# Optimization experiments

Measured on AMD Instinct MI355X. Metric: run time of the kernel, lower is better.

## Reference

```python
import jax, jax.numpy as jnp
import numpy as np

N = 50000      # nodes
E = 800000     # edges (avg degree 16)
HID = 64       # hidden / out_channels per head (concat=False)
EDIM = 3       # edge_dim
H = 4          # heads
C = 64         # per-head channels (== hidden since concat=False mean)
L = 2          # ode_layers
NEG_SLOPE = 0.2
LN_EPS = 1e-5


def setup_inputs() -> dict:
    key = jax.random.key(0)
    ks = jax.random.split(key, 12)
    h = jax.random.normal(ks[0], (N, HID), dtype=jnp.float32)
    edge_index = jax.random.randint(ks[1], (2, E), 0, N, dtype=jnp.int64)
    edge_attr = jax.random.normal(ks[2], (E, EDIM), dtype=jnp.float32)
    t = jnp.zeros((), dtype=jnp.float32)
    s = 1.0 / np.sqrt(HID)
    lin_W = jax.random.normal(ks[3], (L, H * C, HID), dtype=jnp.float32) * s
    lin_W = lin_W.at[L - 1].mul(0.1)  # mimics gats[-1].lin.weight.mul_(0.1)
    lin_edge_W = jax.random.normal(ks[4], (L, H * C, EDIM), dtype=jnp.float32) * (1.0 / np.sqrt(EDIM))
    att_src = jax.random.normal(ks[5], (L, H, C), dtype=jnp.float32) * s
    att_dst = jax.random.normal(ks[6], (L, H, C), dtype=jnp.float32) * s
    att_edge = jax.random.normal(ks[7], (L, H, C), dtype=jnp.float32) * s
    bias = jnp.zeros((L, C), dtype=jnp.float32)
    ln_gamma = jnp.ones((L, HID), dtype=jnp.float32)
    ln_beta = jnp.zeros((L, HID), dtype=jnp.float32)
    return {"t": t, "h": h, "edge_index": edge_index, "edge_attr": edge_attr,
            "lin_W": lin_W, "lin_edge_W": lin_edge_W, "att_src": att_src,
            "att_dst": att_dst, "att_edge": att_edge, "bias": bias,
            "ln_gamma": ln_gamma, "ln_beta": ln_beta}


def _gat_layer(z, src, dst, lin_W, lin_edge_W, att_src, att_dst, att_edge,
               bias, edge_attr):
    n = z.shape[0]
    x = (z @ lin_W.T).reshape(n, H, C)                      # [N,H,C]
    a_src = (x * att_src).sum(-1)                            # [N,H]
    a_dst = (x * att_dst).sum(-1)                            # [N,H]
    e = (edge_attr @ lin_edge_W.T).reshape(-1, H, C)         # [E,H,C]
    a_e = (e * att_edge).sum(-1)                             # [E,H]
    alpha = jax.nn.leaky_relu(a_src[src] + a_dst[dst] + a_e, NEG_SLOPE)
    # segment-softmax over incoming edges of each destination node
    amax = jax.ops.segment_max(alpha, dst, num_segments=n)
    amax = jnp.where(jnp.isfinite(amax), amax, 0.0)
    ex = jnp.exp(alpha - amax[dst])                          # [E,H]
    denom = jax.ops.segment_sum(ex, dst, num_segments=n)
    w = ex / (denom[dst] + 1e-16)
    msg = jax.ops.segment_sum(w[:, :, None] * x[src], dst, num_segments=n)
    return msg.mean(axis=1) + bias                           # [N,C] (concat=False)


def reference(t, h, edge_index, edge_attr, lin_W, lin_edge_W, att_src,
              att_dst, att_edge, bias, ln_gamma, ln_beta):
    src, dst = edge_index[0], edge_index[1]
    z = h
    for i in range(L):
        out = _gat_layer(z, src, dst, lin_W[i], lin_edge_W[i], att_src[i],
                         att_dst[i], att_edge[i], bias[i], edge_attr)
        mu = out.mean(-1, keepdims=True)
        var = ((out - mu) ** 2).mean(-1, keepdims=True)
        ln = (out - mu) / jnp.sqrt(var + LN_EPS) * ln_gamma[i] + ln_beta[i]
        z = jax.nn.silu(ln)
    return z
```

## Files before the change

### kernel.cpp

```cpp
#include <hip/hip_runtime.h>
#include <math.h>

#define NN 50000
#define NE 800000
#define NEG_SLOPE 0.2f
#define LN_EPS 1e-5f
#define SROW 264

typedef unsigned short ushort_t;
typedef unsigned int uint_t;
typedef __attribute__((ext_vector_type(8))) short bf16x8;
typedef __attribute__((ext_vector_type(4))) float f32x4;

__device__ __forceinline__ float bf2f(ushort_t u) {
    return __uint_as_float(((uint_t)u) << 16);
}
__device__ __forceinline__ ushort_t f2bf(float f) {
    uint_t b = __float_as_uint(f);
    uint_t r = (b + 0x7fffu + ((b >> 16) & 1u)) >> 16;
    return (ushort_t)r;
}
__device__ __forceinline__ float ldx(const void* p, size_t i, int isbf) {
    return isbf ? bf2f(((const ushort_t*)p)[i]) : ((const float*)p)[i];
}
__device__ __forceinline__ int clampN(int v) {
    return v < 0 ? 0 : (v >= NN ? NN - 1 : v);
}
__device__ __forceinline__ int ld_src(const int* ei, int e, int f64) {
    return clampN(f64 ? ei[2 * e] : ei[e]);
}
__device__ __forceinline__ int ld_dst(const int* ei, int e, int f64) {
    return clampN(f64 ? ei[2 * NE + 2 * e] : ei[NE + e]);
}
__device__ __forceinline__ int sniff_isbf(const void* hptr) {
    const ushort_t* hu = (const ushort_t*)hptr;
    int bf = 1;
    for (int i = 0; i < 512; i += 2) {
        uint_t ex = (hu[i] >> 7) & 0xFFu;
        if (ex > 0x8Cu) bf = 0;
    }
    return bf;
}
__device__ __forceinline__ int sniff_f64(const int* ei) {
    return (ei[1] == 0 && ei[3] == 0 && ei[5] == 0 && ei[7] == 0) ? 1 : 0;
}

__global__ __launch_bounds__(256) void setup(
    const void* __restrict__ lin_W, const void* __restrict__ lin_edge_W,
    const void* __restrict__ att_src, const void* __restrict__ att_dst,
    const void* __restrict__ att_edge, const void* __restrict__ h_in,
    const int* __restrict__ ei, float* __restrict__ Mbuf,
    ushort_t* __restrict__ wext, ushort_t* __restrict__ hbf,
    int* __restrict__ deg, int* __restrict__ flags) {
    int tid = threadIdx.x, lane = tid & 63;
    int nthreads = gridDim.x * 256;
    int gtid = blockIdx.x * 256 + tid;
    __shared__ int s_isbf;
    if (tid == 0) s_isbf = sniff_isbf(h_in);
    __syncthreads();
    int isbf = s_isbf;
    if (gtid == 0) {
        flags[0] = sniff_f64(ei);
        flags[1] = isbf;
    }
    for (int i = gtid; i < NN; i += nthreads) deg[i] = 0;
    if (blockIdx.x == 0) {
        for (int rep = 0; rep < 2; ++rep) {
            int idx = rep * 256 + tid;
            int l = idx >> 8, hc = idx & 255;
            float ae = ldx(att_edge, l * 256 + hc, isbf);
            size_t b3 = ((size_t)l * 256 + hc) * 3;
            float q0 = ae * ldx(lin_edge_W, b3 + 0, isbf);
            float q1 = ae * ldx(lin_edge_W, b3 + 1, isbf);
            float q2 = ae * ldx(lin_edge_W, b3 + 2, isbf);
            for (int off = 32; off > 0; off >>= 1) {
                q0 += __shfl_down(q0, off);
                q1 += __shfl_down(q1, off);
                q2 += __shfl_down(q2, off);
            }
            if (lane == 0) {
                int h = (idx >> 6) & 3;
                Mbuf[(l * 4 + h) * 3 + 0] = q0;
                Mbuf[(l * 4 + h) * 3 + 1] = q1;
                Mbuf[(l * 4 + h) * 3 + 2] = q2;
            }
        }
    }
    for (int idx = gtid; idx < 2 * 272 * 64; idx += nthreads) {
        int d = idx & 63;
        int row = (idx >> 6) % 272;
        int l = idx / (272 * 64);
        float v = 0.f;
        if (row < 256) {
            v = ldx(lin_W, ((size_t)l * 256 + row) * 64 + d, isbf);
        } else if (row < 264) {
            int h = (row - 256) & 3;
            const void* att = (row < 260) ? att_src : att_dst;
            for (int c = 0; c < 64; ++c) {
                v += ldx(lin_W, ((size_t)l * 256 + h * 64 + c) * 64 + d, isbf) *
                     ldx(att, l * 256 + h * 64 + c, isbf);
            }
        }
        wext[((size_t)l * 272 + row) * 64 + d] = f2bf(v);
    }
    if (!isbf) {
        for (int i = gtid; i < NN * 64; i += nthreads)
            hbf[i] = f2bf(((const float*)h_in)[i]);
    }
}


__global__ void csr_hist_pos(const int* __restrict__ ei, int* __restrict__ deg,
                             int* __restrict__ pos, const int* __restrict__ flags) {
    int e = blockIdx.x * 256 + threadIdx.x;
    if (e >= NE) return;
    pos[e] = atomicAdd(&deg[ld_dst(ei, e, flags[0])], 1);
}

__global__ __launch_bounds__(1024) void csr_scan1(const int* __restrict__ deg,
                                                  int* __restrict__ rowptr,
                                                  int* __restrict__ bsum) {
    __shared__ int sh[1024];
    int i = blockIdx.x * 1024 + threadIdx.x;
    int v = (i < NN) ? deg[i] : 0;
    sh[threadIdx.x] = v;
    __syncthreads();
    for (int off = 1; off < 1024; off <<= 1) {
        int t = (threadIdx.x >= off) ? sh[threadIdx.x - off] : 0;
        __syncthreads();
        sh[threadIdx.x] += t;
        __syncthreads();
    }
    if (i < NN) rowptr[i] = sh[threadIdx.x] - v;
    if (threadIdx.x == 1023) bsum[blockIdx.x] = sh[1023];
}

__global__ __launch_bounds__(1024) void csr_scan23(int* __restrict__ rowptr,
                                                   const int* __restrict__ bsum,
                                                   int nb) {
    __shared__ int off_sh;
    int tid = threadIdx.x;
    if (tid < 64) {
        int v = (tid < blockIdx.x && tid < nb) ? bsum[tid] : 0;
        for (int off = 32; off > 0; off >>= 1) v += __shfl_down(v, off);
        if (tid == 0) off_sh = v;
    }
    __syncthreads();
    int i = blockIdx.x * 1024 + tid;
    if (i < NN) rowptr[i] += off_sh;
    if (i == 0) rowptr[NN] = NE;
}

__global__ void csr_fill(const int* __restrict__ ei, const void* __restrict__ edge_attr,
                         const int* __restrict__ rowptr, const int* __restrict__ pos,
                         float4* __restrict__ edata, const int* __restrict__ flags) {
    int e = blockIdx.x * 256 + threadIdx.x;
    if (e >= NE) return;
    int f64 = flags[0], isbf = flags[1];
    int s = ld_src(ei, e, f64), d = ld_dst(ei, e, f64);
    float4 ed;
    ed.x = ldx(edge_attr, (size_t)e * 3 + 0, isbf);
    ed.y = ldx(edge_attr, (size_t)e * 3 + 1, isbf);
    ed.z = ldx(edge_attr, (size_t)e * 3 + 2, isbf);
    ed.w = __int_as_float(s);
    edata[rowptr[d] + pos[e]] = ed;
}


__global__ __launch_bounds__(256) void node_linear(
    const void* __restrict__ h_in, const ushort_t* __restrict__ hbf,
    const ushort_t* __restrict__ zbuf, const ushort_t* __restrict__ wext,
    ushort_t* __restrict__ xb, float* __restrict__ a_src, float* __restrict__ a_dst,
    const int* __restrict__ flags, int layer) {
    __shared__ __align__(16) ushort_t st_all[4 * 16 * SROW];
    int isbf = flags[1];
    int tid = threadIdx.x, wv = tid >> 6, lane = tid & 63;
    int q = lane >> 4, mi = lane & 15;
    const ushort_t* zsrc = (layer == 0) ? (isbf ? (const ushort_t*)h_in : hbf) : zbuf;
    const ushort_t* wl = wext + (size_t)layer * 272 * 64;
    bf16x8 wf[34];
#pragma unroll
    for (int t = 0; t < 17; ++t) {
        const ushort_t* wrow = wl + (size_t)(t * 16 + mi) * 64;
        wf[2 * t]     = *(const bf16x8*)(wrow + q * 8);
        wf[2 * t + 1] = *(const bf16x8*)(wrow + 32 + q * 8);
    }
    ushort_t* st = st_all + wv * 16 * SROW;
    int gwave = blockIdx.x * 4 + wv, nwaves = gridDim.x * 4;
    for (int tile = gwave; tile < NN / 16; tile += nwaves) {
        int mbase = tile * 16, mynode = mbase + mi;
        const ushort_t* zrow = zsrc + (size_t)mynode * 64;
        bf16x8 b0 = *(const bf16x8*)(zrow + q * 8);
        bf16x8 b1 = *(const bf16x8*)(zrow + 32 + q * 8);
#pragma unroll
        for (int t = 0; t < 17; ++t) {
            f32x4 acc = {0.f, 0.f, 0.f, 0.f};
            acc = __builtin_amdgcn_mfma_f32_16x16x32_bf16(wf[2 * t], b0, acc, 0, 0, 0);
            acc = __builtin_amdgcn_mfma_f32_16x16x32_bf16(wf[2 * t + 1], b1, acc, 0, 0, 0);
            if (t < 16) {
                ushort4 pk;
                pk.x = f2bf(acc[0]);
                pk.y = f2bf(acc[1]);
                pk.z = f2bf(acc[2]);
                pk.w = f2bf(acc[3]);
                *(ushort4*)(st + mi * SROW + t * 16 + q * 4) = pk;
            } else {
                float4 av;
                av.x = acc[0]; av.y = acc[1]; av.z = acc[2]; av.w = acc[3];
                if (q == 0) *(float4*)(a_src + (size_t)mynode * 4) = av;
                else if (q == 1) *(float4*)(a_dst + (size_t)mynode * 4) = av;
            }
        }
        for (int nn = 0; nn < 16; ++nn) {
            int node = mbase + nn;
            ushort4 pk;
            pk.x = st[nn * SROW + lane];
            pk.y = st[nn * SROW + 64 + lane];
            pk.z = st[nn * SROW + 128 + lane];
            pk.w = st[nn * SROW + 192 + lane];
            *(ushort4*)(xb + (size_t)node * 256 + lane * 4) = pk;
        }
    }
}

__global__ __launch_bounds__(256) void node_aggregate(
    const int* __restrict__ rowptr, const float4* __restrict__ edata,
    const float* __restrict__ a_src, const float* __restrict__ a_dst,
    const ushort_t* __restrict__ xb, const float* __restrict__ Mbuf,
    const void* __restrict__ bias, const void* __restrict__ gamma,
    const void* __restrict__ beta, ushort_t* __restrict__ zout,
    void* __restrict__ outp, const int* __restrict__ flags, int layer, int last) {
    __shared__ float4 wsh[4][64];
    __shared__ int ssh[4][64];
    int isbf = flags[1];
    int wv = threadIdx.x >> 6;
    int lane = threadIdx.x & 63;
    int n = blockIdx.x * 4 + wv;
    float M[12];
#pragma unroll
    for (int i = 0; i < 12; ++i) M[i] = Mbuf[layer * 12 + i];
    float4 ad = *(const float4*)(a_dst + (size_t)n * 4);
    int start = rowptr[n], end = rowptr[n + 1];
    float acc0 = 0.f, acc1 = 0.f, acc2 = 0.f, acc3 = 0.f;
    float den0 = 0.f, den1 = 0.f, den2 = 0.f, den3 = 0.f;
    for (int cb = start; cb < end; cb += 64) {
        int m = end - cb;
        if (m > 64) m = 64;
        if (lane < m) {
            float4 ed = edata[cb + lane];
            int s = __float_as_int(ed.w);
            float4 as4 = *(const float4*)(a_src + (size_t)s * 4);
            float t0 = as4.x + ad.x + ed.x * M[0] + ed.y * M[1] + ed.z * M[2];
            float t1 = as4.y + ad.y + ed.x * M[3] + ed.y * M[4] + ed.z * M[5];
            float t2 = as4.z + ad.z + ed.x * M[6] + ed.y * M[7] + ed.z * M[8];
            float t3 = as4.w + ad.w + ed.x * M[9] + ed.y * M[10] + ed.z * M[11];
            t0 = t0 > 0.f ? t0 : NEG_SLOPE * t0;
            t1 = t1 > 0.f ? t1 : NEG_SLOPE * t1;
            t2 = t2 > 0.f ? t2 : NEG_SLOPE * t2;
            t3 = t3 > 0.f ? t3 : NEG_SLOPE * t3;
            float4 ex;
            ex.x = __expf(fminf(t0, 80.f));
            ex.y = __expf(fminf(t1, 80.f));
            ex.z = __expf(fminf(t2, 80.f));
            ex.w = __expf(fminf(t3, 80.f));
            wsh[wv][lane] = ex;
            ssh[wv][lane] = s;
        }
        for (int j = 0; j < m; j += 4) {
            int j1 = j + 1 < m ? j + 1 : m - 1;
            int j2 = j + 2 < m ? j + 2 : m - 1;
            int j3 = j + 3 < m ? j + 3 : m - 1;
            int s0 = ssh[wv][j],  s1 = ssh[wv][j1];
            int s2 = ssh[wv][j2], s3 = ssh[wv][j3];
            float4 w0 = wsh[wv][j];
            float4 w1 = wsh[wv][j1];
            float4 w2 = wsh[wv][j2];
            float4 w3 = wsh[wv][j3];
            if (j + 1 >= m) w1 = make_float4(0.f, 0.f, 0.f, 0.f);
            if (j + 2 >= m) w2 = make_float4(0.f, 0.f, 0.f, 0.f);
            if (j + 3 >= m) w3 = make_float4(0.f, 0.f, 0.f, 0.f);
            ushort4 x0 = *(const ushort4*)(xb + (size_t)s0 * 256 + lane * 4);
            ushort4 x1 = *(const ushort4*)(xb + (size_t)s1 * 256 + lane * 4);
            ushort4 x2 = *(const ushort4*)(xb + (size_t)s2 * 256 + lane * 4);
            ushort4 x3 = *(const ushort4*)(xb + (size_t)s3 * 256 + lane * 4);
            acc0 += w0.x * bf2f(x0.x) + w1.x * bf2f(x1.x) +
                    w2.x * bf2f(x2.x) + w3.x * bf2f(x3.x);
            acc1 += w0.y * bf2f(x0.y) + w1.y * bf2f(x1.y) +
                    w2.y * bf2f(x2.y) + w3.y * bf2f(x3.y);
            acc2 += w0.z * bf2f(x0.z) + w1.z * bf2f(x1.z) +
                    w2.z * bf2f(x2.z) + w3.z * bf2f(x3.z);
            acc3 += w0.w * bf2f(x0.w) + w1.w * bf2f(x1.w) +
                    w2.w * bf2f(x2.w) + w3.w * bf2f(x3.w);
            den0 += w0.x + w1.x + w2.x + w3.x;
            den1 += w0.y + w1.y + w2.y + w3.y;
            den2 += w0.z + w1.z + w2.z + w3.z;
            den3 += w0.w + w1.w + w2.w + w3.w;
        }
    }
    float v = ldx(bias, layer * 64 + lane, isbf) +
              0.25f * (acc0 / (den0 + 1e-16f) + acc1 / (den1 + 1e-16f) +
                       acc2 / (den2 + 1e-16f) + acc3 / (den3 + 1e-16f));
    float sum = v;
    for (int off = 1; off < 64; off <<= 1) sum += __shfl_xor(sum, off);
    float mu = sum * (1.f / 64.f);
    float d = v - mu;
    float vv = d * d;
    for (int off = 1; off < 64; off <<= 1) vv += __shfl_xor(vv, off);
    float var = vv * (1.f / 64.f);
    float ln = d * rsqrtf(var + LN_EPS) * ldx(gamma, layer * 64 + lane, isbf) +
               ldx(beta, layer * 64 + lane, isbf);
    float sl = ln / (1.f + __expf(-ln));
    size_t idx = (size_t)n * 64 + lane;
    if (last) {
        if (isbf) ((ushort_t*)outp)[idx] = f2bf(sl);
        else      ((float*)outp)[idx] = sl;
    } else {
        zout[idx] = f2bf(sl);
    }
}

extern "C" void kernel_launch(void* const* d_in, const int* in_sizes, int n_in,
                              void* d_out, int out_size, void* d_ws, size_t ws_size,
                              hipStream_t stream) {
    int off = (in_sizes[0] == 1) ? 1 : 0;
    const void* h_in  = d_in[off + 0];
    const int*  ei    = (const int*)d_in[off + 1];
    const void* eattr = d_in[off + 2];
    const void* linW  = d_in[off + 3];
    const void* linEW = d_in[off + 4];
    const void* attS  = d_in[off + 5];
    const void* attD  = d_in[off + 6];
    const void* attE  = d_in[off + 7];
    const void* bias  = d_in[off + 8];
    const void* gamma = d_in[off + 9];
    const void* beta  = d_in[off + 10];

    char* w = (char*)d_ws;
    size_t o = 0;
    auto alloc = [&](size_t bytes) {
        void* q = w + o;
        o += (bytes + 255) & ~(size_t)255;
        return q;
    };
    int*    flags  = (int*)alloc(8);
    float*  Mbuf   = (float*)alloc(24 * 4);
    ushort_t* wext = (ushort_t*)alloc((size_t)2 * 272 * 64 * 2);
    float*  a_src  = (float*)alloc((size_t)NN * 4 * 4);
    float*  a_dst  = (float*)alloc((size_t)NN * 4 * 4);
    int*    rowptr = (int*)alloc((size_t)(NN + 1) * 4);
    int*    deg    = (int*)alloc((size_t)NN * 4);
    int*    pos    = (int*)alloc((size_t)NE * 4);
    int*    bsum   = (int*)alloc(256 * 4);
    ushort_t* zbuf = (ushort_t*)alloc((size_t)NN * 64 * 2);
    ushort_t* hbf  = (ushort_t*)alloc((size_t)NN * 64 * 2);
    ushort_t* xb   = (ushort_t*)alloc((size_t)NN * 256 * 2);
    float4* edata  = (float4*)alloc((size_t)NE * 16);

    int nb = (NN + 1023) / 1024;
    setup<<<256, 256, 0, stream>>>(linW, linEW, attS, attD, attE, h_in, ei,
                                   Mbuf, wext, hbf, deg, flags);
    csr_hist_pos<<<(NE + 255) / 256, 256, 0, stream>>>(ei, deg, pos, flags);
    csr_scan1<<<nb, 1024, 0, stream>>>(deg, rowptr, bsum);
    csr_scan23<<<nb, 1024, 0, stream>>>(rowptr, bsum, nb);
    csr_fill<<<(NE + 255) / 256, 256, 0, stream>>>(ei, eattr, rowptr, pos, edata, flags);

    for (int l = 0; l < 2; ++l) {
        node_linear<<<512, 256, 0, stream>>>(h_in, hbf, zbuf, wext, xb,
                                             a_src, a_dst, flags, l);
        node_aggregate<<<NN / 4, 256, 0, stream>>>(rowptr, edata, a_src, a_dst,
                                                   xb, Mbuf, bias, gamma, beta,
                                                   zbuf, d_out, flags, l, l == 1);
    }
}
```

Before: 329.9 us.

## Make node_aggregate lanes own one head's 4 contiguous channels

Changes the xb layout from channel-interleaved to head-major contiguous by writing rows with a vector LDS read. In node_aggregate, each lane now handles one head and 4 consecutive channels, so it needs one softmax weight per edge instead of four. The per-edge weights and pre-shifted source offsets are staged in LDS as grouped quads, read with vector loads, accumulated with FMAs, and the heads are reduced through cross-lane shuffles. This is meant to cut per-edge ALU and LDS traffic and the tail masking work, at the cost of extra shuffles and output writes done by only a quarter of the lanes.

```diff
diff --git a/kernel.cpp b/kernel.cpp
--- a/kernel.cpp
+++ b/kernel.cpp
@@ -213,11 +213,7 @@
         }
         for (int nn = 0; nn < 16; ++nn) {
             int node = mbase + nn;
-            ushort4 pk;
-            pk.x = st[nn * SROW + lane];
-            pk.y = st[nn * SROW + 64 + lane];
-            pk.z = st[nn * SROW + 128 + lane];
-            pk.w = st[nn * SROW + 192 + lane];
+            ushort4 pk = *(const ushort4*)(st + nn * SROW + lane * 4);
             *(ushort4*)(xb + (size_t)node * 256 + lane * 4) = pk;
         }
     }
@@ -230,24 +226,29 @@
     const void* __restrict__ bias, const void* __restrict__ gamma,
     const void* __restrict__ beta, ushort_t* __restrict__ zout,
     void* __restrict__ outp, const int* __restrict__ flags, int layer, int last) {
-    __shared__ float4 wsh[4][64];
-    __shared__ int ssh[4][64];
+    __shared__ __align__(16) float wq[4][16][4][4];
+    __shared__ __align__(16) int sq[4][16][4];
     int isbf = flags[1];
     int wv = threadIdx.x >> 6;
     int lane = threadIdx.x & 63;
+    int hidx = lane >> 4;
+    int ch0 = (lane & 15) << 2;
+    int loff = ((hidx << 6) + ch0) << 1;
     int n = blockIdx.x * 4 + wv;
     float M[12];
 #pragma unroll
     for (int i = 0; i < 12; ++i) M[i] = Mbuf[layer * 12 + i];
     float4 ad = *(const float4*)(a_dst + (size_t)n * 4);
     int start = rowptr[n], end = rowptr[n + 1];
+    const char* xbc = (const char*)xb;
     float acc0 = 0.f, acc1 = 0.f, acc2 = 0.f, acc3 = 0.f;
-    float den0 = 0.f, den1 = 0.f, den2 = 0.f, den3 = 0.f;
+    float den = 0.f;
     for (int cb = start; cb < end; cb += 64) {
         int m = end - cb;
         if (m > 64) m = 64;
-        if (lane < m) {
-            float4 ed = edata[cb + lane];
+        {
+            int le = lane < m ? lane : 0;
+            float4 ed = edata[cb + le];
             int s = __float_as_int(ed.w);
             float4 as4 = *(const float4*)(a_src + (size_t)s * 4);
             float t0 = as4.x + ad.x + ed.x * M[0] + ed.y * M[1] + ed.z * M[2];
@@ -258,64 +259,94 @@
             t1 = t1 > 0.f ? t1 : NEG_SLOPE * t1;
             t2 = t2 > 0.f ? t2 : NEG_SLOPE * t2;
             t3 = t3 > 0.f ? t3 : NEG_SLOPE * t3;
-            float4 ex;
-            ex.x = __expf(fminf(t0, 80.f));
-            ex.y = __expf(fminf(t1, 80.f));
-            ex.z = __expf(fminf(t2, 80.f));
-            ex.w = __expf(fminf(t3, 80.f));
-            wsh[wv][lane] = ex;
-            ssh[wv][lane] = s;
-        }
-        for (int j = 0; j < m; j += 4) {
-            int j1 = j + 1 < m ? j + 1 : m - 1;
-            int j2 = j + 2 < m ? j + 2 : m - 1;
-            int j3 = j + 3 < m ? j + 3 : m - 1;
-            int s0 = ssh[wv][j],  s1 = ssh[wv][j1];
-            int s2 = ssh[wv][j2], s3 = ssh[wv][j3];
-            float4 w0 = wsh[wv][j];
-            float4 w1 = wsh[wv][j1];
-            float4 w2 = wsh[wv][j2];
-            float4 w3 = wsh[wv][j3];
-            if (j + 1 >= m) w1 = make_float4(0.f, 0.f, 0.f, 0.f);
-            if (j + 2 >= m) w2 = make_float4(0.f, 0.f, 0.f, 0.f);
-            if (j + 3 >= m) w3 = make_float4(0.f, 0.f, 0.f, 0.f);
-            ushort4 x0 = *(const ushort4*)(xb + (size_t)s0 * 256 + lane * 4);
-            ushort4 x1 = *(const ushort4*)(xb + (size_t)s1 * 256 + lane * 4);
-            ushort4 x2 = *(const ushort4*)(xb + (size_t)s2 * 256 + lane * 4);
-            ushort4 x3 = *(const ushort4*)(xb + (size_t)s3 * 256 + lane * 4);
-            acc0 += w0.x * bf2f(x0.x) + w1.x * bf2f(x1.x) +
-                    w2.x * bf2f(x2.x) + w3.x * bf2f(x3.x);
-            acc1 += w0.y * bf2f(x0.y) + w1.y * bf2f(x1.y) +
-                    w2.y * bf2f(x2.y) + w3.y * bf2f(x3.y);
-            acc2 += w0.z * bf2f(x0.z) + w1.z * bf2f(x1.z) +
-                    w2.z * bf2f(x2.z) + w3.z * bf2f(x3.z);
-            acc3 += w0.w * bf2f(x0.w) + w1.w * bf2f(x1.w) +
-                    w2.w * bf2f(x2.w) + w3.w * bf2f(x3.w);
-            den0 += w0.x + w1.x + w2.x + w3.x;
-            den1 += w0.y + w1.y + w2.y + w3.y;
-            den2 += w0.z + w1.z + w2.z + w3.z;
-            den3 += w0.w + w1.w + w2.w + w3.w;
-        }
-    }
-    float v = ldx(bias, layer * 64 + lane, isbf) +
-              0.25f * (acc0 / (den0 + 1e-16f) + acc1 / (den1 + 1e-16f) +
-                       acc2 / (den2 + 1e-16f) + acc3 / (den3 + 1e-16f));
-    float sum = v;
-    for (int off = 1; off < 64; off <<= 1) sum += __shfl_xor(sum, off);
-    float mu = sum * (1.f / 64.f);
-    float d = v - mu;
-    float vv = d * d;
-    for (int off = 1; off < 64; off <<= 1) vv += __shfl_xor(vv, off);
-    float var = vv * (1.f / 64.f);
-    float ln = d * rsqrtf(var + LN_EPS) * ldx(gamma, layer * 64 + lane, isbf) +
-               ldx(beta, layer * 64 + lane, isbf);
-    float sl = ln / (1.f + __expf(-ln));
-    size_t idx = (size_t)n * 64 + lane;
-    if (last) {
-        if (isbf) ((ushort_t*)outp)[idx] = f2bf(sl);
-        else      ((float*)outp)[idx] = sl;
-    } else {
-        zout[idx] = f2bf(sl);
+            float e0 = __expf(fminf(t0, 80.f));
+            float e1 = __expf(fminf(t1, 80.f));
+            float e2 = __expf(fminf(t2, 80.f));
+            float e3 = __expf(fminf(t3, 80.f));
+            if (lane >= m) { e0 = 0.f; e1 = 0.f; e2 = 0.f; e3 = 0.f; s = 0; }
+            int jq = lane >> 2, r = lane & 3;
+            sq[wv][jq][r] = s << 9;
+            wq[wv][jq][0][r] = e0;
+            wq[wv][jq][1][r] = e1;
+            wq[wv][jq][2][r] = e2;
+            wq[wv][jq][3][r] = e3;
+        }
+        int mq = (m + 3) >> 2;
+        for (int j = 0; j < mq; ++j) {
+            float4 w4 = *(const float4*)&wq[wv][j][hidx][0];
+            int4 s4 = *(const int4*)&sq[wv][j][0];
+            ushort4 x0 = *(const ushort4*)(xbc + (size_t)(unsigned)(s4.x + loff));
+            ushort4 x1 = *(const ushort4*)(xbc + (size_t)(unsigned)(s4.y + loff));
+            ushort4 x2 = *(const ushort4*)(xbc + (size_t)(unsigned)(s4.z + loff));
+            ushort4 x3 = *(const ushort4*)(xbc + (size_t)(unsigned)(s4.w + loff));
+            acc0 = fmaf(w4.x, bf2f(x0.x), acc0);
+            acc1 = fmaf(w4.x, bf2f(x0.y), acc1);
+            acc2 = fmaf(w4.x, bf2f(x0.z), acc2);
+            acc3 = fmaf(w4.x, bf2f(x0.w), acc3);
+            acc0 = fmaf(w4.y, bf2f(x1.x), acc0);
+            acc1 = fmaf(w4.y, bf2f(x1.y), acc1);
+            acc2 = fmaf(w4.y, bf2f(x1.z), acc2);
+            acc3 = fmaf(w4.y, bf2f(x1.w), acc3);
+            acc0 = fmaf(w4.z, bf2f(x2.x), acc0);
+            acc1 = fmaf(w4.z, bf2f(x2.y), acc1);
+            acc2 = fmaf(w4.z, bf2f(x2.z), acc2);
+            acc3 = fmaf(w4.z, bf2f(x2.w), acc3);
+            acc0 = fmaf(w4.w, bf2f(x3.x), acc0);
+            acc1 = fmaf(w4.w, bf2f(x3.y), acc1);
+            acc2 = fmaf(w4.w, bf2f(x3.z), acc2);
+            acc3 = fmaf(w4.w, bf2f(x3.w), acc3);
+            den += (w4.x + w4.y) + (w4.z + w4.w);
+        }
+    }
+    float inv = 1.f / (den + 1e-16f);
+    float v0 = acc0 * inv, v1 = acc1 * inv, v2 = acc2 * inv, v3 = acc3 * inv;
+    v0 += __shfl_xor(v0, 16); v0 += __shfl_xor(v0, 32);
+    v1 += __shfl_xor(v1, 16); v1 += __shfl_xor(v1, 32);
+    v2 += __shfl_xor(v2, 16); v2 += __shfl_xor(v2, 32);
+    v3 += __shfl_xor(v3, 16); v3 += __shfl_xor(v3, 32);
+    size_t pb = (size_t)layer * 64 + ch0;
+    v0 = ldx(bias, pb + 0, isbf) + 0.25f * v0;
+    v1 = ldx(bias, pb + 1, isbf) + 0.25f * v1;
+    v2 = ldx(bias, pb + 2, isbf) + 0.25f * v2;
+    v3 = ldx(bias, pb + 3, isbf) + 0.25f * v3;
+    float lsum = (v0 + v1) + (v2 + v3);
+    lsum += __shfl_xor(lsum, 1);
+    lsum += __shfl_xor(lsum, 2);
+    lsum += __shfl_xor(lsum, 4);
+    lsum += __shfl_xor(lsum, 8);
+    float mu = lsum * (1.f / 64.f);
+    float d0 = v0 - mu, d1 = v1 - mu, d2 = v2 - mu, d3 = v3 - mu;
+    float ss = (d0 * d0 + d1 * d1) + (d2 * d2 + d3 * d3);
+    ss += __shfl_xor(ss, 1);
+    ss += __shfl_xor(ss, 2);
+    ss += __shfl_xor(ss, 4);
+    ss += __shfl_xor(ss, 8);
+    float rstd = rsqrtf(ss * (1.f / 64.f) + LN_EPS);
+    float l0 = d0 * rstd * ldx(gamma, pb + 0, isbf) + ldx(beta, pb + 0, isbf);
+    float l1 = d1 * rstd * ldx(gamma, pb + 1, isbf) + ldx(beta, pb + 1, isbf);
+    float l2 = d2 * rstd * ldx(gamma, pb + 2, isbf) + ldx(beta, pb + 2, isbf);
+    float l3 = d3 * rstd * ldx(gamma, pb + 3, isbf) + ldx(beta, pb + 3, isbf);
+    float s0 = l0 / (1.f + __expf(-l0));
+    float s1 = l1 / (1.f + __expf(-l1));
+    float s2 = l2 / (1.f + __expf(-l2));
+    float s3 = l3 / (1.f + __expf(-l3));
+    if (hidx == 0) {
+        size_t base = (size_t)n * 64 + ch0;
+        if (last) {
+            if (isbf) {
+                ushort4 pk;
+                pk.x = f2bf(s0); pk.y = f2bf(s1); pk.z = f2bf(s2); pk.w = f2bf(s3);
+                *(ushort4*)((ushort_t*)outp + base) = pk;
+            } else {
+                float4 fv;
+                fv.x = s0; fv.y = s1; fv.z = s2; fv.w = s3;
+                *(float4*)((float*)outp + base) = fv;
+            }
+        } else {
+            ushort4 pk;
+            pk.x = f2bf(s0); pk.y = f2bf(s1); pk.z = f2bf(s2); pk.w = f2bf(s3);
+            *(ushort4*)(zout + base) = pk;
+        }
     }
 }
 
```

After: 355.2 us. 7.7% more time.

## Compact edge indices in setup and fuse f32-to-bf16 input conversion into node_linear

Applied to the files above, without the earlier changes.

The setup kernel now decodes edge_index once into compact int32 src/dst arrays with vectorized loads, so the histogram and fill kernels read dense 4-byte indices instead of strided int64 words. The separate pass converting h to a bf16 buffer is removed, and layer-0 node_linear converts f32 rows to bf16 in registers. The dtype sniff is also parallelized across the block instead of running in one thread. This adds an extra 6.4 MB of index writes in setup.

```diff
diff --git a/kernel.cpp b/kernel.cpp
--- a/kernel.cpp
+++ b/kernel.cpp
@@ -26,21 +26,6 @@
 __device__ __forceinline__ int clampN(int v) {
     return v < 0 ? 0 : (v >= NN ? NN - 1 : v);
 }
-__device__ __forceinline__ int ld_src(const int* ei, int e, int f64) {
-    return clampN(f64 ? ei[2 * e] : ei[e]);
-}
-__device__ __forceinline__ int ld_dst(const int* ei, int e, int f64) {
-    return clampN(f64 ? ei[2 * NE + 2 * e] : ei[NE + e]);
-}
-__device__ __forceinline__ int sniff_isbf(const void* hptr) {
-    const ushort_t* hu = (const ushort_t*)hptr;
-    int bf = 1;
-    for (int i = 0; i < 512; i += 2) {
-        uint_t ex = (hu[i] >> 7) & 0xFFu;
-        if (ex > 0x8Cu) bf = 0;
-    }
-    return bf;
-}
 __device__ __forceinline__ int sniff_f64(const int* ei) {
     return (ei[1] == 0 && ei[3] == 0 && ei[5] == 0 && ei[7] == 0) ? 1 : 0;
 }
@@ -50,20 +35,47 @@
     const void* __restrict__ att_src, const void* __restrict__ att_dst,
     const void* __restrict__ att_edge, const void* __restrict__ h_in,
     const int* __restrict__ ei, float* __restrict__ Mbuf,
-    ushort_t* __restrict__ wext, ushort_t* __restrict__ hbf,
+    ushort_t* __restrict__ wext, int* __restrict__ esrc, int* __restrict__ edst,
     int* __restrict__ deg, int* __restrict__ flags) {
     int tid = threadIdx.x, lane = tid & 63;
     int nthreads = gridDim.x * 256;
     int gtid = blockIdx.x * 256 + tid;
-    __shared__ int s_isbf;
-    if (tid == 0) s_isbf = sniff_isbf(h_in);
+    __shared__ int s_bf;
+    if (tid == 0) s_bf = 1;
     __syncthreads();
-    int isbf = s_isbf;
+    {
+        uint_t ex = (((const ushort_t*)h_in)[2 * tid] >> 7) & 0xFFu;
+        if (ex > 0x8Cu) s_bf = 0;
+    }
+    __syncthreads();
+    int isbf = s_bf;
+    int f64 = sniff_f64(ei);
     if (gtid == 0) {
-        flags[0] = sniff_f64(ei);
+        flags[0] = f64;
         flags[1] = isbf;
     }
     for (int i = gtid; i < NN; i += nthreads) deg[i] = 0;
+    if (f64) {
+        const int4* s4 = (const int4*)ei;
+        const int4* d4 = (const int4*)(ei + 2 * NE);
+        for (int p = gtid; p < NE / 2; p += nthreads) {
+            int4 sv = s4[p], dv = d4[p];
+            esrc[2 * p]     = clampN(sv.x);
+            esrc[2 * p + 1] = clampN(sv.z);
+            edst[2 * p]     = clampN(dv.x);
+            edst[2 * p + 1] = clampN(dv.z);
+        }
+    } else {
+        const int2* s2 = (const int2*)ei;
+        const int2* d2 = (const int2*)(ei + NE);
+        for (int p = gtid; p < NE / 2; p += nthreads) {
+            int2 sv = s2[p], dv = d2[p];
+            esrc[2 * p]     = clampN(sv.x);
+            esrc[2 * p + 1] = clampN(sv.y);
+            edst[2 * p]     = clampN(dv.x);
+            edst[2 * p + 1] = clampN(dv.y);
+        }
+    }
     if (blockIdx.x == 0) {
         for (int rep = 0; rep < 2; ++rep) {
             int idx = rep * 256 + tid;
@@ -103,18 +115,14 @@
         }
         wext[((size_t)l * 272 + row) * 64 + d] = f2bf(v);
     }
-    if (!isbf) {
-        for (int i = gtid; i < NN * 64; i += nthreads)
-            hbf[i] = f2bf(((const float*)h_in)[i]);
-    }
-}
-
-
-__global__ void csr_hist_pos(const int* __restrict__ ei, int* __restrict__ deg,
-                             int* __restrict__ pos, const int* __restrict__ flags) {
+}
+
+
+__global__ void csr_hist_pos(const int* __restrict__ edst, int* __restrict__ deg,
+                             int* __restrict__ pos) {
     int e = blockIdx.x * 256 + threadIdx.x;
     if (e >= NE) return;
-    pos[e] = atomicAdd(&deg[ld_dst(ei, e, flags[0])], 1);
+    pos[e] = atomicAdd(&deg[edst[e]], 1);
 }
 
 __global__ __launch_bounds__(1024) void csr_scan1(const int* __restrict__ deg,
@@ -151,13 +159,14 @@
     if (i == 0) rowptr[NN] = NE;
 }
 
-__global__ void csr_fill(const int* __restrict__ ei, const void* __restrict__ edge_attr,
+__global__ void csr_fill(const int* __restrict__ esrc, const int* __restrict__ edst,
+                         const void* __restrict__ edge_attr,
                          const int* __restrict__ rowptr, const int* __restrict__ pos,
                          float4* __restrict__ edata, const int* __restrict__ flags) {
     int e = blockIdx.x * 256 + threadIdx.x;
     if (e >= NE) return;
-    int f64 = flags[0], isbf = flags[1];
-    int s = ld_src(ei, e, f64), d = ld_dst(ei, e, f64);
+    int isbf = flags[1];
+    int s = esrc[e], d = edst[e];
     float4 ed;
     ed.x = ldx(edge_attr, (size_t)e * 3 + 0, isbf);
     ed.y = ldx(edge_attr, (size_t)e * 3 + 1, isbf);
@@ -168,15 +177,16 @@
 
 
 __global__ __launch_bounds__(256) void node_linear(
-    const void* __restrict__ h_in, const ushort_t* __restrict__ hbf,
-    const ushort_t* __restrict__ zbuf, const ushort_t* __restrict__ wext,
+    const void* __restrict__ h_in, const ushort_t* __restrict__ zbuf,
+    const ushort_t* __restrict__ wext,
     ushort_t* __restrict__ xb, float* __restrict__ a_src, float* __restrict__ a_dst,
     const int* __restrict__ flags, int layer) {
     __shared__ __align__(16) ushort_t st_all[4 * 16 * SROW];
     int isbf = flags[1];
     int tid = threadIdx.x, wv = tid >> 6, lane = tid & 63;
     int q = lane >> 4, mi = lane & 15;
-    const ushort_t* zsrc = (layer == 0) ? (isbf ? (const ushort_t*)h_in : hbf) : zbuf;
+    int f32path = (layer == 0) && !isbf;
+    const ushort_t* zsrc = (layer == 0) ? (const ushort_t*)h_in : zbuf;
     const ushort_t* wl = wext + (size_t)layer * 272 * 64;
     bf16x8 wf[34];
 #pragma unroll
@@ -189,9 +199,26 @@
     int gwave = blockIdx.x * 4 + wv, nwaves = gridDim.x * 4;
     for (int tile = gwave; tile < NN / 16; tile += nwaves) {
         int mbase = tile * 16, mynode = mbase + mi;
-        const ushort_t* zrow = zsrc + (size_t)mynode * 64;
-        bf16x8 b0 = *(const bf16x8*)(zrow + q * 8);
-        bf16x8 b1 = *(const bf16x8*)(zrow + 32 + q * 8);
+        bf16x8 b0, b1;
+        if (f32path) {
+            const float* zf = (const float*)h_in + (size_t)mynode * 64;
+            float4 fa = *(const float4*)(zf + q * 8);
+            float4 fb = *(const float4*)(zf + q * 8 + 4);
+            float4 fc = *(const float4*)(zf + 32 + q * 8);
+            float4 fd = *(const float4*)(zf + 32 + q * 8 + 4);
+            b0[0] = (short)f2bf(fa.x); b0[1] = (short)f2bf(fa.y);
+            b0[2] = (short)f2bf(fa.z); b0[3] = (short)f2bf(fa.w);
+            b0[4] = (short)f2bf(fb.x); b0[5] = (short)f2bf(fb.y);
+            b0[6] = (short)f2bf(fb.z); b0[7] = (short)f2bf(fb.w);
+            b1[0] = (short)f2bf(fc.x); b1[1] = (short)f2bf(fc.y);
+            b1[2] = (short)f2bf(fc.z); b1[3] = (short)f2bf(fc.w);
+            b1[4] = (short)f2bf(fd.x); b1[5] = (short)f2bf(fd.y);
+            b1[6] = (short)f2bf(fd.z); b1[7] = (short)f2bf(fd.w);
+        } else {
+            const ushort_t* zrow = zsrc + (size_t)mynode * 64;
+            b0 = *(const bf16x8*)(zrow + q * 8);
+            b1 = *(const bf16x8*)(zrow + 32 + q * 8);
+        }
 #pragma unroll
         for (int t = 0; t < 17; ++t) {
             f32x4 acc = {0.f, 0.f, 0.f, 0.f};
@@ -352,20 +379,22 @@
     int*    pos    = (int*)alloc((size_t)NE * 4);
     int*    bsum   = (int*)alloc(256 * 4);
     ushort_t* zbuf = (ushort_t*)alloc((size_t)NN * 64 * 2);
-    ushort_t* hbf  = (ushort_t*)alloc((size_t)NN * 64 * 2);
+    int*    esrc   = (int*)alloc((size_t)NE * 4);
+    int*    edst   = (int*)alloc((size_t)NE * 4);
     ushort_t* xb   = (ushort_t*)alloc((size_t)NN * 256 * 2);
     float4* edata  = (float4*)alloc((size_t)NE * 16);
 
     int nb = (NN + 1023) / 1024;
     setup<<<256, 256, 0, stream>>>(linW, linEW, attS, attD, attE, h_in, ei,
-                                   Mbuf, wext, hbf, deg, flags);
-    csr_hist_pos<<<(NE + 255) / 256, 256, 0, stream>>>(ei, deg, pos, flags);
+                                   Mbuf, wext, esrc, edst, deg, flags);
+    csr_hist_pos<<<(NE + 255) / 256, 256, 0, stream>>>(edst, deg, pos);
     csr_scan1<<<nb, 1024, 0, stream>>>(deg, rowptr, bsum);
     csr_scan23<<<nb, 1024, 0, stream>>>(rowptr, bsum, nb);
-    csr_fill<<<(NE + 255) / 256, 256, 0, stream>>>(ei, eattr, rowptr, pos, edata, flags);
+    csr_fill<<<(NE + 255) / 256, 256, 0, stream>>>(esrc, edst, eattr, rowptr,
+                                                   pos, edata, flags);
 
     for (int l = 0; l < 2; ++l) {
-        node_linear<<<512, 256, 0, stream>>>(h_in, hbf, zbuf, wext, xb,
+        node_linear<<<512, 256, 0, stream>>>(h_in, zbuf, wext, xb,
                                              a_src, a_dst, flags, l);
         node_aggregate<<<NN / 4, 256, 0, stream>>>(rowptr, edata, a_src, a_dst,
                                                    xb, Mbuf, bias, gamma, beta,
```

Result: faster. 313.8 us (-4.9%).
